# Kernel optimization log

Hardware: AMD Instinct MI355X
Metric: run time of the kernel (lower is better)

## Reference

```python
import jax, jax.numpy as jnp
import numpy as np

TOP_K = 4

def setup_inputs() -> dict:
    key = jax.random.key(0)
    ks = jax.random.split(key, 10)
    s = 0.02
    return {
        "x": jax.random.normal(ks[0], (4, 1024, 2048), jnp.float32),
        "expert_bias": jnp.zeros((64,), jnp.float32),
        "router_w": jax.random.normal(ks[1], (64, 2048), jnp.float32) * s,
        "gate_w": jax.random.normal(ks[2], (8192, 2048), jnp.float32) * s,
        "up_w": jax.random.normal(ks[3], (8192, 2048), jnp.float32) * s,
        "down_w": jax.random.normal(ks[4], (2048, 8192), jnp.float32) * s,
        "w_down": jax.random.normal(ks[5], (512, 2048), jnp.float32) * s,
        "w_up": jax.random.normal(ks[6], (2048, 512), jnp.float32) * s,
        "experts_w12": jax.random.normal(ks[7], (64, 512, 2048), jnp.float32) * s,
        "experts_w3": jax.random.normal(ks[8], (64, 1024, 512), jnp.float32) * s,
    }


def reference(x, expert_bias, router_w, gate_w, up_w, down_w, w_down, w_up, experts_w12, experts_w3):
    B, S, D = x.shape
    E = router_w.shape[0]
    K = TOP_K
    h = x.reshape(-1, D)            # [N, D]
    N = h.shape[0]
    NK = N * K

    # --- router (fp32) ---
    logits = h @ router_w.T          # [N, E]
    scores = jax.nn.sigmoid(logits)
    z_loss = jnp.mean(logits * logits) * 1e-4
    sel = scores + expert_bias
    _, topk_idx = jax.lax.top_k(sel, K)                      # [N, K]
    topk_logits = jnp.take_along_axis(logits, topk_idx, axis=1)
    gating = jax.nn.softmax(topk_logits, axis=-1)            # [N, K]

    # --- shared SwiGLU expert ---
    shared = (jax.nn.silu(h @ gate_w.T) * (h @ up_w.T)) @ down_w.T   # [N, D]

    # --- bottleneck down projection ---
    hd = h @ w_down.T                # [N, bottle]
    Bn = hd.shape[1]

    # --- dispatch: sort tokens by expert, capacity max_load per expert ---
    flat = topk_idx.reshape(-1)                      # [NK]
    perm = jnp.argsort(flat)                         # stable sort
    sorted_e = flat[perm]
    counts = jnp.bincount(flat, length=E)
    ptr = jnp.cumsum(counts) - counts                # start offset per expert
    local = jnp.arange(NK) - ptr[sorted_e]           # rank within expert
    max_load = (NK // E // 8 + 6) * 8                # static python int
    num_slots = E * max_load
    mask = local < max_load
    slots = sorted_e * max_load + local
    tok = jnp.repeat(jnp.arange(N), K)               # token id per routed slot

    # reverse_map[slot] = token index (N = dummy)
    rm = jnp.full((num_slots + 1,), N, dtype=jnp.int32)
    rm = rm.at[jnp.where(mask, slots, num_slots)].set(tok[perm].astype(jnp.int32))
    reverse_map = rm[:num_slots]

    hwd = jnp.concatenate([hd, jnp.zeros((1, Bn), hd.dtype)], axis=0)
    padding = hwd[reverse_map].reshape(E, max_load, Bn)

    # --- grouped expert GEMMs ---
    h12 = jnp.einsum('emb,ebf->emf', padding, experts_w12)   # [E, L, 2*F]
    h1, h2 = jnp.split(h12, 2, axis=-1)
    pout = jnp.einsum('emf,efb->emb', jax.nn.silu(h1) * h2, experts_w3)
    pout = pout.reshape(-1, Bn)                              # [num_slots, bottle]

    # --- combine: gather back per (token, k) slot and mix with gating ---
    powd = jnp.concatenate([pout, jnp.zeros((1, Bn), pout.dtype)], axis=0)
    gm = jnp.full((NK + 1,), num_slots, dtype=jnp.int32)
    gm = gm.at[jnp.where(mask, perm, NK)].set(jnp.where(mask, slots, num_slots).astype(jnp.int32))
    gather_map = gm[:NK]
    gathered = powd[gather_map].reshape(N, K, Bn)
    routed_b = jnp.einsum('nk,nkb->nb', gating, gathered)
    routed = routed_b @ w_up.T                               # [N, D]

    # eval mode: route_scale = 1.0, moe_scale = 0.5 (one shared expert), aux_loss = 0
    out = (shared + routed) * 0.5
    return out.reshape(B, S, D), z_loss
```

## Files before the change

kernel.cpp:

```cpp
#include <hip/hip_runtime.h>
#include <math.h>

#define NTOK 4096
#define DMODEL 2048
#define ENUM 64
#define HSH 8192
#define BND 512
#define FEXP 1024
#define MAXL 304
#define EPAD 384
#define ECH 16

typedef float f32x4 __attribute__((ext_vector_type(4)));
using bf16x8 = __attribute__((ext_vector_type(8))) __bf16;

typedef const __attribute__((address_space(1))) unsigned int cgu32;
typedef __attribute__((address_space(3))) unsigned int lu32;
#define GLOAD16(g, l) __builtin_amdgcn_global_load_lds((cgu32*)(g), (lu32*)(l), 16, 0, 0)

__device__ __forceinline__ unsigned short f2bf(float f) {
    union { float f; unsigned int u; } v; v.f = f;
    unsigned int u = v.u;
    return (unsigned short)((u + 0x7FFFu + ((u >> 16) & 1u)) >> 16);
}
__device__ __forceinline__ float bf2f(unsigned short s) {
    union { unsigned int u; float f; } v; v.u = ((unsigned int)s) << 16;
    return v.f;
}

__global__ __launch_bounds__(256) void init_kernel(float* zacc, int* slot2tok, unsigned short* hdz) {
    int i = blockIdx.x * 256 + threadIdx.x;
    if (i == 0) *zacc = 0.f;
    if (i < ENUM * MAXL) slot2tok[i] = NTOK;
    if (i < BND) hdz[i] = 0;
}

__global__ __launch_bounds__(256) void convert_kernel(
    const float* __restrict__ in, unsigned short* __restrict__ out, long long n)
{
    long long stride = (long long)gridDim.x * 256 * 8;
    for (long long i = ((long long)blockIdx.x * 256 + threadIdx.x) * 8; i < n; i += stride) {
        float4 a = *(const float4*)(in + i);
        float4 b = *(const float4*)(in + i + 4);
        union { unsigned short s[8]; uint4 v; } o;
        o.s[0] = f2bf(a.x); o.s[1] = f2bf(a.y); o.s[2] = f2bf(a.z); o.s[3] = f2bf(a.w);
        o.s[4] = f2bf(b.x); o.s[5] = f2bf(b.y); o.s[6] = f2bf(b.z); o.s[7] = f2bf(b.w);
        *(uint4*)(out + i) = o.v;
    }
}

__global__ __launch_bounds__(256) void convert_x_kernel(
    const float* __restrict__ in, unsigned short* __restrict__ hi,
    unsigned short* __restrict__ lo, long long n)
{
    long long stride = (long long)gridDim.x * 256 * 8;
    for (long long i = ((long long)blockIdx.x * 256 + threadIdx.x) * 8; i < n; i += stride) {
        float4 a = *(const float4*)(in + i);
        float4 b = *(const float4*)(in + i + 4);
        union { unsigned short s[8]; uint4 v; } oh, ol;
        float f[8] = {a.x, a.y, a.z, a.w, b.x, b.y, b.z, b.w};
#pragma unroll
        for (int j = 0; j < 8; j++) {
            unsigned short h = f2bf(f[j]);
            oh.s[j] = h;
            ol.s[j] = f2bf(f[j] - bf2f(h));
        }
        *(uint4*)(hi + i) = oh.v;
        *(uint4*)(lo + i) = ol.v;
    }
}

__global__ __launch_bounds__(256) void convert_rw_kernel(
    const float* __restrict__ rw, unsigned short* __restrict__ whi,
    unsigned short* __restrict__ wlo)
{
    int i = (blockIdx.x * 256 + threadIdx.x) * 4;
    if (i >= 128 * 2048) return;
    ushort4 oh = {0, 0, 0, 0}, ol = {0, 0, 0, 0};
    if (i < 64 * 2048) {
        float4 f = *(const float4*)(rw + i);
        float v[4] = {f.x, f.y, f.z, f.w};
        unsigned short h;
        h = f2bf(v[0]); oh.x = h; ol.x = f2bf(v[0] - bf2f(h));
        h = f2bf(v[1]); oh.y = h; ol.y = f2bf(v[1] - bf2f(h));
        h = f2bf(v[2]); oh.z = h; ol.z = f2bf(v[2] - bf2f(h));
        h = f2bf(v[3]); oh.w = h; ol.w = f2bf(v[3] - bf2f(h));
    }
    *(ushort4*)(whi + i) = oh;
    *(ushort4*)(wlo + i) = ol;
}

__global__ __launch_bounds__(256) void tconv_kernel(
    const float* __restrict__ in, unsigned short* __restrict__ out, int Kd, int Nd)
{
    __shared__ float t[32][33];
    size_t zoff = (size_t)blockIdx.z * Kd * Nd;
    in += zoff; out += zoff;
    int n0 = blockIdx.x * 32, k0 = blockIdx.y * 32;
    int r = threadIdx.x >> 3, c = (threadIdx.x & 7) * 4;
    float4 v = *(const float4*)(in + (size_t)(k0 + r) * Nd + n0 + c);
    t[r][c] = v.x; t[r][c + 1] = v.y; t[r][c + 2] = v.z; t[r][c + 3] = v.w;
    __syncthreads();
    ushort4 o;
    o.x = f2bf(t[c + 0][r]); o.y = f2bf(t[c + 1][r]);
    o.z = f2bf(t[c + 2][r]); o.w = f2bf(t[c + 3][r]);
    *(ushort4*)(out + (size_t)(n0 + r) * Kd + k0 + c) = o;
}

__global__ __launch_bounds__(256) void rgemm_kernel(
    const unsigned short* __restrict__ xb, const unsigned short* __restrict__ xlo,
    const unsigned short* __restrict__ whi, const unsigned short* __restrict__ wlo,
    float* __restrict__ logits)
{
    __shared__ unsigned short As[2][128 * 64];
    __shared__ unsigned short Bs[2][128 * 64];
    const int z = blockIdx.z;
    const int m0 = blockIdx.y * 128;
    const int tid = threadIdx.x;
    const int lane = tid & 63;
    const int w = tid >> 6;
    const int wm = (w >> 1) * 64;
    const int wn = (w & 1) * 64;

    const unsigned short* Ab = (z == 2) ? xlo : xb;
    const unsigned short* Bb = (z == 1) ? wlo : whi;
    float* Cb = logits + (size_t)z * NTOK * 128;

    size_t asrc[4], bsrc[4];
    int ldso[4];
#pragma unroll
    for (int i = 0; i < 4; i++) {
        int u = i * 256 + tid;
        int r = u >> 3;
        int ce = ((u & 7) ^ (r & 7)) * 8;
        ldso[i] = u * 8;
        asrc[i] = (size_t)(m0 + r) * DMODEL + ce;
        bsrc[i] = (size_t)r * DMODEL + ce;
    }

    const int lrow = lane & 15;
    const int kg = lane >> 4;
    const int mk = (lrow & 7) << 4;
    int arx[4], brx[4];
#pragma unroll
    for (int t = 0; t < 4; t++) {
        arx[t] = (wm + t * 16 + lrow) * 128;
        brx[t] = (wn + t * 16 + lrow) * 128;
    }

    f32x4 acc[4][4];
#pragma unroll
    for (int a = 0; a < 4; a++)
#pragma unroll
        for (int b = 0; b < 4; b++) acc[a][b] = (f32x4)0.f;

#pragma unroll
    for (int i = 0; i < 4; i++) GLOAD16(Ab + asrc[i], &As[0][ldso[i]]);
#pragma unroll
    for (int i = 0; i < 4; i++) GLOAD16(Bb + bsrc[i], &Bs[0][ldso[i]]);
#pragma unroll
    for (int i = 0; i < 4; i++) GLOAD16(Ab + asrc[i] + 64, &As[1][ldso[i]]);
#pragma unroll
    for (int i = 0; i < 4; i++) GLOAD16(Bb + bsrc[i] + 64, &Bs[1][ldso[i]]);

    const int nt = DMODEL >> 6;
    int cur = 0;
    for (int t = 0; t < nt; ++t) {
        if (t + 1 < nt) asm volatile("s_waitcnt vmcnt(8)" ::: "memory");
        else            asm volatile("s_waitcnt vmcnt(0)" ::: "memory");
        __builtin_amdgcn_s_barrier();
        __builtin_amdgcn_sched_barrier(0);
        const char* Abase = (const char*)&As[cur][0];
        const char* Bbase = (const char*)&Bs[cur][0];
#pragma unroll
        for (int ks = 0; ks < 2; ks++) {
            const int cb = (ks * 64 + kg * 16) ^ mk;
            bf16x8 a[4], b[4];
#pragma unroll
            for (int t2 = 0; t2 < 4; t2++) {
                a[t2] = *(const bf16x8*)(Abase + arx[t2] + cb);
                b[t2] = *(const bf16x8*)(Bbase + brx[t2] + cb);
            }
#pragma unroll
            for (int ni = 0; ni < 4; ni++)
#pragma unroll
                for (int mi = 0; mi < 4; mi++)
                    acc[mi][ni] = __builtin_amdgcn_mfma_f32_16x16x32_bf16(a[mi], b[ni], acc[mi][ni], 0, 0, 0);
        }
        __builtin_amdgcn_sched_barrier(0);
        asm volatile("s_waitcnt lgkmcnt(0)" ::: "memory");
        __builtin_amdgcn_s_barrier();
        __builtin_amdgcn_sched_barrier(0);
        const int kn = (t + 2) * 64;
        if (kn < DMODEL) {
#pragma unroll
            for (int i = 0; i < 4; i++) GLOAD16(Ab + asrc[i] + kn, &As[cur][ldso[i]]);
#pragma unroll
            for (int i = 0; i < 4; i++) GLOAD16(Bb + bsrc[i] + kn, &Bs[cur][ldso[i]]);
        }
        cur ^= 1;
    }

    const int rb0 = m0 + wm + (kg << 2);
#pragma unroll
    for (int mi = 0; mi < 4; mi++)
#pragma unroll
        for (int ni = 0; ni < 4; ni++) {
            int col = wn + ni * 16 + lrow;
#pragma unroll
            for (int r = 0; r < 4; r++)
                Cb[(size_t)(rb0 + mi * 16 + r) * 128 + col] = acc[mi][ni][r];
        }
}

__global__ __launch_bounds__(256) void topk_kernel(
    const float* __restrict__ logits, const float* __restrict__ bias,
    int* __restrict__ topk_idx, float* __restrict__ gating, float* __restrict__ zacc)
{
    __shared__ float zpart[4];
    const size_t Z = (size_t)NTOK * 128;
    int wv = threadIdx.x >> 6, lane = threadIdx.x & 63;
    int n = blockIdx.x * 4 + wv;
    const float* lp = logits + (size_t)n * 128 + lane;
    float logit = lp[0] + lp[Z] + lp[2 * Z];
    float sel = 1.f / (1.f + expf(-logit)) + bias[lane];
    float zsq = logit * logit;
    for (int off = 32; off; off >>= 1) zsq += __shfl_down(zsq, off);
    if (lane == 0) zpart[wv] = zsq;
    __syncthreads();
    if (threadIdx.x == 0) atomicAdd(zacc, zpart[0] + zpart[1] + zpart[2] + zpart[3]);
    float cur = sel;
    float ch_logit[4]; int ch_idx[4];
    for (int kk = 0; kk < 4; kk++) {
        float v = cur; int idx = lane;
        for (int off = 1; off < 64; off <<= 1) {
            float v2 = __shfl_xor(v, off);
            int i2 = __shfl_xor(idx, off);
            if (v2 > v || (v2 == v && i2 < idx)) { v = v2; idx = i2; }
        }
        ch_idx[kk] = idx;
        ch_logit[kk] = __shfl(logit, idx);
        if (lane == idx) cur = -1e30f;
    }
    if (lane == 0) {
        float mx = ch_logit[0];
        for (int kk = 1; kk < 4; kk++) mx = fmaxf(mx, ch_logit[kk]);
        float se = 0.f, ex[4];
        for (int kk = 0; kk < 4; kk++) { ex[kk] = expf(ch_logit[kk] - mx); se += ex[kk]; }
        for (int kk = 0; kk < 4; kk++) {
            topk_idx[n * 4 + kk] = ch_idx[kk];
            gating[n * 4 + kk] = ex[kk] / se;
        }
    }
}

__global__ __launch_bounds__(256) void rank_kernel(
    const int* __restrict__ topk_idx, int* __restrict__ slot2tok, int* __restrict__ gmap)
{
    int e = blockIdx.x;
    __shared__ int wsum[4];
    int tid = threadIdx.x;
    int lane = tid & 63, w = tid >> 6;
    int running = 0;
    for (int c = 0; c < NTOK * 4; c += 256) {
        int i = c + tid;
        int fl = topk_idx[i];
        bool m = (fl == e);
        unsigned long long bal = __ballot(m);
        int prefix = __popcll(bal & ((1ULL << lane) - 1ULL));
        if (lane == 0) wsum[w] = __popcll(bal);
        __syncthreads();
        int wbase = 0;
        for (int j = 0; j < w; j++) wbase += wsum[j];
        int total = wsum[0] + wsum[1] + wsum[2] + wsum[3];
        if (m) {
            int rank = running + wbase + prefix;
            int tok = i >> 2;
            if (rank < MAXL) {
                slot2tok[e * MAXL + rank] = tok;
                gmap[i] = e * MAXL + rank;
            } else gmap[i] = -1;
        }
        running += total;
        __syncthreads();
    }
}

template<int GATHER, int EPI>
__global__ __launch_bounds__(256) void gemm2(
    const unsigned short* __restrict__ A, long long aZ, int lda,
    const int* __restrict__ gtab,
    const unsigned short* __restrict__ Bm, long long bZ, int ldb,
    void* __restrict__ Cb, long long cZ, int ldc,
    int M, int K)
{
    __shared__ unsigned short As[2][128 * 64];
    __shared__ unsigned short Bs[2][128 * 64];
    const int z = blockIdx.z;
    const int m0 = blockIdx.y * 128;
    const int n0 = blockIdx.x * 128;
    const int tid = threadIdx.x;
    const int lane = tid & 63;
    const int w = tid >> 6;
    const int wm = (w >> 1) * 64;
    const int wn = (w & 1) * 64;

    const unsigned short* Ab = A + (GATHER ? (size_t)0 : (size_t)z * aZ);
    const unsigned short* Bb = Bm + (size_t)z * bZ;

    size_t asrc[4], bsrc[4];
    int ldso[4];
#pragma unroll
    for (int i = 0; i < 4; i++) {
        int u = i * 256 + tid;
        int r = u >> 3;
        int ce = ((u & 7) ^ (r & 7)) * 8;
        ldso[i] = u * 8;
        if constexpr (GATHER) {
            int mr = m0 + r;
            int tok = (mr < M) ? gtab[(size_t)z * MAXL + mr] : NTOK;
            asrc[i] = (size_t)tok * lda + ce;
        } else {
            asrc[i] = (size_t)(m0 + r) * lda + ce;
        }
        bsrc[i] = (size_t)(n0 + r) * ldb + ce;
    }

    const int lrow = lane & 15;
    const int kg = lane >> 4;
    const int mk = (lrow & 7) << 4;
    int arx[4], brx[4];
#pragma unroll
    for (int t = 0; t < 4; t++) {
        arx[t] = (wm + t * 16 + lrow) * 128;
        brx[t] = (wn + t * 16 + lrow) * 128;
    }

    f32x4 acc[4][4];
#pragma unroll
    for (int a = 0; a < 4; a++)
#pragma unroll
        for (int b = 0; b < 4; b++) acc[a][b] = (f32x4)0.f;

#pragma unroll
    for (int i = 0; i < 4; i++) GLOAD16(Ab + asrc[i], &As[0][ldso[i]]);
#pragma unroll
    for (int i = 0; i < 4; i++) GLOAD16(Bb + bsrc[i], &Bs[0][ldso[i]]);
    if (64 < K) {
#pragma unroll
        for (int i = 0; i < 4; i++) GLOAD16(Ab + asrc[i] + 64, &As[1][ldso[i]]);
#pragma unroll
        for (int i = 0; i < 4; i++) GLOAD16(Bb + bsrc[i] + 64, &Bs[1][ldso[i]]);
    }

    const int nt = K >> 6;
    int cur = 0;
    for (int t = 0; t < nt; ++t) {
        if (t + 1 < nt) asm volatile("s_waitcnt vmcnt(8)" ::: "memory");
        else            asm volatile("s_waitcnt vmcnt(0)" ::: "memory");
        __builtin_amdgcn_s_barrier();
        __builtin_amdgcn_sched_barrier(0);
        const char* Abase = (const char*)&As[cur][0];
        const char* Bbase = (const char*)&Bs[cur][0];
#pragma unroll
        for (int ks = 0; ks < 2; ks++) {
            const int cb = (ks * 64 + kg * 16) ^ mk;
            bf16x8 a[4], b[4];
#pragma unroll
            for (int t2 = 0; t2 < 4; t2++) {
                a[t2] = *(const bf16x8*)(Abase + arx[t2] + cb);
                b[t2] = *(const bf16x8*)(Bbase + brx[t2] + cb);
            }
#pragma unroll
            for (int ni = 0; ni < 4; ni++)
#pragma unroll
                for (int mi = 0; mi < 4; mi++)
                    acc[mi][ni] = __builtin_amdgcn_mfma_f32_16x16x32_bf16(a[mi], b[ni], acc[mi][ni], 0, 0, 0);
        }
        __builtin_amdgcn_sched_barrier(0);
        asm volatile("s_waitcnt lgkmcnt(0)" ::: "memory");
        __builtin_amdgcn_s_barrier();
        __builtin_amdgcn_sched_barrier(0);
        const int kn = (t + 2) * 64;
        if (kn < K) {
#pragma unroll
            for (int i = 0; i < 4; i++) GLOAD16(Ab + asrc[i] + kn, &As[cur][ldso[i]]);
#pragma unroll
            for (int i = 0; i < 4; i++) GLOAD16(Bb + bsrc[i] + kn, &Bs[cur][ldso[i]]);
        }
        cur ^= 1;
    }

    const int rb0 = m0 + wm + (kg << 2);
#pragma unroll
    for (int mi = 0; mi < 4; mi++)
#pragma unroll
        for (int ni = 0; ni < 4; ni++) {
            int col = n0 + wn + ni * 16 + lrow;
#pragma unroll
            for (int r = 0; r < 4; r++) {
                int row = rb0 + mi * 16 + r;
                if (row < M) {
                    size_t ci = (size_t)z * cZ + (size_t)row * ldc + col;
                    float v = acc[mi][ni][r];
                    if constexpr (EPI == 0) {
                        ((unsigned short*)Cb)[ci] = f2bf(v);
                    } else if constexpr (EPI == 1) {
                        unsigned short* cp = (unsigned short*)Cb + ci;
                        float g = bf2f(*cp);
                        *cp = f2bf(g / (1.f + expf(-g)) * v);
                    } else if constexpr (EPI == 2) {
                        ((float*)Cb)[ci] = v;
                    } else {
                        float* cp = (float*)Cb + ci;
                        *cp = (*cp + v) * 0.5f;
                    }
                }
            }
        }
}

__global__ __launch_bounds__(256) void siluact_kernel(
    const unsigned short* __restrict__ h12, unsigned short* __restrict__ act)
{
    int e = blockIdx.y, m = blockIdx.x;
    const unsigned short* hr = h12 + ((size_t)e * EPAD + m) * 2048;
    unsigned short* ar = act + ((size_t)e * EPAD + m) * 1024;
    int j = threadIdx.x * 4;
    ushort4 h1 = *(const ushort4*)(hr + j);
    ushort4 h2 = *(const ushort4*)(hr + 1024 + j);
    ushort4 o;
    float v;
    v = bf2f(h1.x); o.x = f2bf(v / (1.f + expf(-v)) * bf2f(h2.x));
    v = bf2f(h1.y); o.y = f2bf(v / (1.f + expf(-v)) * bf2f(h2.y));
    v = bf2f(h1.z); o.z = f2bf(v / (1.f + expf(-v)) * bf2f(h2.z));
    v = bf2f(h1.w); o.w = f2bf(v / (1.f + expf(-v)) * bf2f(h2.w));
    *(ushort4*)(ar + j) = o;
}

__global__ __launch_bounds__(256) void gather_kernel(
    const unsigned short* __restrict__ pout, const int* __restrict__ gmap,
    const float* __restrict__ gating, unsigned short* __restrict__ routed_b)
{
    int n = blockIdx.x;
    int j = threadIdx.x * 2;
    float a0 = 0.f, a1 = 0.f;
#pragma unroll
    for (int kk = 0; kk < 4; kk++) {
        int slot = gmap[n * 4 + kk];
        float g = gating[n * 4 + kk];
        if (slot >= 0) {
            const unsigned short* pr = pout + (size_t)slot * BND + j;
            a0 += g * bf2f(pr[0]);
            a1 += g * bf2f(pr[1]);
        }
    }
    routed_b[(size_t)n * BND + j] = f2bf(a0);
    routed_b[(size_t)n * BND + j + 1] = f2bf(a1);
}

__global__ void zloss_kernel(const float* zacc, float* out) {
    out[0] = zacc[0] * (1.0e-4f / (float)(NTOK * ENUM));
}

extern "C" void kernel_launch(void* const* d_in, const int* in_sizes, int n_in,
                              void* d_out, int out_size, void* d_ws, size_t ws_size,
                              hipStream_t stream)
{
    const float* x      = (const float*)d_in[0];
    const float* ebias  = (const float*)d_in[1];
    const float* rw     = (const float*)d_in[2];
    const float* gate_w = (const float*)d_in[3];
    const float* up_w   = (const float*)d_in[4];
    const float* down_w = (const float*)d_in[5];
    const float* w_down = (const float*)d_in[6];
    const float* w_up   = (const float*)d_in[7];
    const float* w12    = (const float*)d_in[8];
    const float* w3     = (const float*)d_in[9];
    float* out = (float*)d_out;

    char* ws = (char*)d_ws;
    size_t off = 0;
    auto alloc = [&](size_t b) { size_t o = off; off += (b + 255) & ~(size_t)255; return o; };
    float* zacc     = (float*)(ws + alloc(4));
    int*   topk     = (int*)(ws + alloc((size_t)NTOK * 4 * 4));
    float* gating   = (float*)(ws + alloc((size_t)NTOK * 4 * 4));
    int*   gmap     = (int*)(ws + alloc((size_t)NTOK * 4 * 4));
    int*   slot2tok = (int*)(ws + alloc((size_t)ENUM * MAXL * 4));
    unsigned short* xb     = (unsigned short*)(ws + alloc((size_t)NTOK * DMODEL * 2));
    unsigned short* hd     = (unsigned short*)(ws + alloc((size_t)(NTOK + 1) * BND * 2));
    unsigned short* rb     = (unsigned short*)(ws + alloc((size_t)NTOK * BND * 2));
    unsigned short* wdownb = (unsigned short*)(ws + alloc((size_t)BND * DMODEL * 2));
    unsigned short* wupb   = (unsigned short*)(ws + alloc((size_t)DMODEL * BND * 2));
    unsigned short* wbuf   = (unsigned short*)(ws + alloc((size_t)HSH * DMODEL * 2));
    unsigned short* H1     = (unsigned short*)(ws + alloc((size_t)NTOK * HSH * 2));
    unsigned short* h12  = H1;
    unsigned short* act  = H1 + (size_t)ECH * EPAD * 2048;
    unsigned short* pout = H1 + (size_t)ECH * EPAD * 2048 + (size_t)ECH * EPAD * 1024;
    unsigned short* xlo    = H1;
    float*          logits = (float*)((char*)H1 + (size_t)NTOK * DMODEL * 2);
    unsigned short* whi    = (unsigned short*)((char*)logits + (size_t)3 * NTOK * 128 * 4);
    unsigned short* wlo    = whi + (size_t)128 * DMODEL;

    init_kernel<<<(ENUM * MAXL + 255) / 256, 256, 0, stream>>>(zacc, slot2tok, hd + (size_t)NTOK * BND);

    convert_x_kernel<<<1024, 256, 0, stream>>>(x, xb, xlo, (long long)NTOK * DMODEL);
    convert_rw_kernel<<<(128 * 2048 / 4 + 255) / 256, 256, 0, stream>>>(rw, whi, wlo);
    rgemm_kernel<<<dim3(1, NTOK / 128, 3), 256, 0, stream>>>(xb, xlo, whi, wlo, logits);
    topk_kernel<<<NTOK / 4, 256, 0, stream>>>(logits, ebias, topk, gating, zacc);
    rank_kernel<<<ENUM, 256, 0, stream>>>(topk, slot2tok, gmap);

    convert_kernel<<<256, 256, 0, stream>>>(w_down, wdownb, (long long)BND * DMODEL);
    convert_kernel<<<256, 256, 0, stream>>>(w_up, wupb, (long long)DMODEL * BND);

    gemm2<0, 0><<<dim3(BND / 128, NTOK / 128, 1), 256, 0, stream>>>(
        xb, 0, DMODEL, nullptr, wdownb, 0, DMODEL, hd, 0, BND, NTOK, DMODEL);

    convert_kernel<<<1024, 256, 0, stream>>>(gate_w, wbuf, (long long)HSH * DMODEL);
    gemm2<0, 0><<<dim3(HSH / 128, NTOK / 128, 1), 256, 0, stream>>>(
        xb, 0, DMODEL, nullptr, wbuf, 0, DMODEL, H1, 0, HSH, NTOK, DMODEL);
    convert_kernel<<<1024, 256, 0, stream>>>(up_w, wbuf, (long long)HSH * DMODEL);
    gemm2<0, 1><<<dim3(HSH / 128, NTOK / 128, 1), 256, 0, stream>>>(
        xb, 0, DMODEL, nullptr, wbuf, 0, DMODEL, H1, 0, HSH, NTOK, DMODEL);
    convert_kernel<<<1024, 256, 0, stream>>>(down_w, wbuf, (long long)DMODEL * HSH);
    gemm2<0, 2><<<dim3(DMODEL / 128, NTOK / 128, 1), 256, 0, stream>>>(
        H1, 0, HSH, nullptr, wbuf, 0, HSH, out, 0, DMODEL, NTOK, HSH);

    for (int c = 0; c < ENUM / ECH; c++) {
        tconv_kernel<<<dim3(2048 / 32, 512 / 32, ECH), 256, 0, stream>>>(
            w12 + (size_t)c * ECH * 512 * 2048, wbuf, 512, 2048);
        gemm2<1, 0><<<dim3(2048 / 128, 3, ECH), 256, 0, stream>>>(
            hd, 0, BND, slot2tok + (size_t)c * ECH * MAXL,
            wbuf, (long long)2048 * 512, 512,
            h12, (long long)EPAD * 2048, 2048, MAXL, BND);
        tconv_kernel<<<dim3(512 / 32, 1024 / 32, ECH), 256, 0, stream>>>(
            w3 + (size_t)c * ECH * 1024 * 512, wbuf, 1024, 512);
        siluact_kernel<<<dim3(EPAD, ECH), 256, 0, stream>>>(h12, act);
        gemm2<0, 0><<<dim3(BND / 128, 3, ECH), 256, 0, stream>>>(
            act, (long long)EPAD * FEXP, FEXP, nullptr,
            wbuf, (long long)BND * FEXP, FEXP,
            pout + (size_t)c * ECH * MAXL * BND, (long long)MAXL * BND, BND, MAXL, FEXP);
    }

    gather_kernel<<<NTOK, 256, 0, stream>>>(pout, gmap, gating, rb);

    gemm2<0, 3><<<dim3(DMODEL / 128, NTOK / 128, 1), 256, 0, stream>>>(
        rb, 0, BND, nullptr, wupb, 0, BND, out, 0, DMODEL, NTOK, BND);

    zloss_kernel<<<1, 1, 0, stream>>>(zacc, out + (size_t)NTOK * DMODEL);
}
```

Baseline: 1.097 ms.

## Fuse shared-expert gate and up GEMMs into one dual-accumulator kernel

Replaces the separate gate GEMM (bf16 store) and up GEMM (read-back plus SiLU epilogue) with a single kernel. It loads one A tile and both gate and up B tiles, keeps two accumulator sets, and writes silu(g)*u directly. This reads the activation tiles once and avoids writing and re-reading the intermediate H1 gate result. Weights are converted in two halves so they fit the existing buffer. The cost is much higher register use (32 f32x4 accumulators) and 48KB of LDS per block, which may lower occupancy.

```diff
diff --git a/kernel.cpp b/kernel.cpp
--- a/kernel.cpp
+++ b/kernel.cpp
@@ -420,6 +420,95 @@
         }
 }
 
+__global__ __launch_bounds__(256) void gemmgu(
+    const unsigned short* __restrict__ A, int lda,
+    const unsigned short* __restrict__ Bg, const unsigned short* __restrict__ Bu,
+    int ldb, unsigned short* __restrict__ H, int ldh, int ncol0, int K)
+{
+    __shared__ unsigned short As[128 * 64];
+    __shared__ unsigned short Bgs[128 * 64];
+    __shared__ unsigned short Bus[128 * 64];
+    const int m0 = blockIdx.y * 128;
+    const int n0 = blockIdx.x * 128;
+    const int tid = threadIdx.x;
+    const int lane = tid & 63;
+    const int w = tid >> 6;
+    const int wm = (w >> 1) * 64;
+    const int wn = (w & 1) * 64;
+
+    size_t asrc[4], bsrc[4];
+    int ldso[4];
+#pragma unroll
+    for (int i = 0; i < 4; i++) {
+        int u = i * 256 + tid;
+        int r = u >> 3;
+        int ce = ((u & 7) ^ (r & 7)) * 8;
+        ldso[i] = u * 8;
+        asrc[i] = (size_t)(m0 + r) * lda + ce;
+        bsrc[i] = (size_t)(n0 + r) * ldb + ce;
+    }
+
+    const int lrow = lane & 15;
+    const int kg = lane >> 4;
+    const int mk = (lrow & 7) << 4;
+    int arx[4], brx[4];
+#pragma unroll
+    for (int t = 0; t < 4; t++) {
+        arx[t] = (wm + t * 16 + lrow) * 128;
+        brx[t] = (wn + t * 16 + lrow) * 128;
+    }
+
+    f32x4 accg[4][4], accu[4][4];
+#pragma unroll
+    for (int a = 0; a < 4; a++)
+#pragma unroll
+        for (int b = 0; b < 4; b++) { accg[a][b] = (f32x4)0.f; accu[a][b] = (f32x4)0.f; }
+
+    for (int k0 = 0; k0 < K; k0 += 64) {
+#pragma unroll
+        for (int i = 0; i < 4; i++) GLOAD16(A + asrc[i] + k0, &As[ldso[i]]);
+#pragma unroll
+        for (int i = 0; i < 4; i++) GLOAD16(Bg + bsrc[i] + k0, &Bgs[ldso[i]]);
+#pragma unroll
+        for (int i = 0; i < 4; i++) GLOAD16(Bu + bsrc[i] + k0, &Bus[ldso[i]]);
+        __syncthreads();
+#pragma unroll
+        for (int ks = 0; ks < 2; ks++) {
+            const int cb = (ks * 64 + kg * 16) ^ mk;
+            bf16x8 a[4], bg[4], bu[4];
+#pragma unroll
+            for (int t2 = 0; t2 < 4; t2++) {
+                a[t2]  = *(const bf16x8*)((const char*)As  + arx[t2] + cb);
+                bg[t2] = *(const bf16x8*)((const char*)Bgs + brx[t2] + cb);
+                bu[t2] = *(const bf16x8*)((const char*)Bus + brx[t2] + cb);
+            }
+#pragma unroll
+            for (int ni = 0; ni < 4; ni++)
+#pragma unroll
+                for (int mi = 0; mi < 4; mi++) {
+                    accg[mi][ni] = __builtin_amdgcn_mfma_f32_16x16x32_bf16(a[mi], bg[ni], accg[mi][ni], 0, 0, 0);
+                    accu[mi][ni] = __builtin_amdgcn_mfma_f32_16x16x32_bf16(a[mi], bu[ni], accu[mi][ni], 0, 0, 0);
+                }
+        }
+        __syncthreads();
+    }
+
+    const int rb0 = m0 + wm + (kg << 2);
+#pragma unroll
+    for (int mi = 0; mi < 4; mi++)
+#pragma unroll
+        for (int ni = 0; ni < 4; ni++) {
+            int col = ncol0 + n0 + wn + ni * 16 + lrow;
+#pragma unroll
+            for (int r = 0; r < 4; r++) {
+                int row = rb0 + mi * 16 + r;
+                float g = accg[mi][ni][r];
+                float u = accu[mi][ni][r];
+                H[(size_t)row * ldh + col] = f2bf(g / (1.f + expf(-g)) * u);
+            }
+        }
+}
+
 __global__ __launch_bounds__(256) void siluact_kernel(
     const unsigned short* __restrict__ h12, unsigned short* __restrict__ act)
 {
@@ -516,12 +605,16 @@
     gemm2<0, 0><<<dim3(BND / 128, NTOK / 128, 1), 256, 0, stream>>>(
         xb, 0, DMODEL, nullptr, wdownb, 0, DMODEL, hd, 0, BND, NTOK, DMODEL);
 
-    convert_kernel<<<1024, 256, 0, stream>>>(gate_w, wbuf, (long long)HSH * DMODEL);
-    gemm2<0, 0><<<dim3(HSH / 128, NTOK / 128, 1), 256, 0, stream>>>(
-        xb, 0, DMODEL, nullptr, wbuf, 0, DMODEL, H1, 0, HSH, NTOK, DMODEL);
-    convert_kernel<<<1024, 256, 0, stream>>>(up_w, wbuf, (long long)HSH * DMODEL);
-    gemm2<0, 1><<<dim3(HSH / 128, NTOK / 128, 1), 256, 0, stream>>>(
-        xb, 0, DMODEL, nullptr, wbuf, 0, DMODEL, H1, 0, HSH, NTOK, DMODEL);
+    for (int half = 0; half < 2; half++) {
+        convert_kernel<<<512, 256, 0, stream>>>(
+            gate_w + (size_t)half * (HSH / 2) * DMODEL, wbuf, (long long)(HSH / 2) * DMODEL);
+        convert_kernel<<<512, 256, 0, stream>>>(
+            up_w + (size_t)half * (HSH / 2) * DMODEL, wbuf + (size_t)(HSH / 2) * DMODEL,
+            (long long)(HSH / 2) * DMODEL);
+        gemmgu<<<dim3((HSH / 2) / 128, NTOK / 128, 1), 256, 0, stream>>>(
+            xb, DMODEL, wbuf, wbuf + (size_t)(HSH / 2) * DMODEL, DMODEL,
+            H1, HSH, half * (HSH / 2), DMODEL);
+    }
     convert_kernel<<<1024, 256, 0, stream>>>(down_w, wbuf, (long long)DMODEL * HSH);
     gemm2<0, 2><<<dim3(DMODEL / 128, NTOK / 128, 1), 256, 0, stream>>>(
         H1, 0, HSH, nullptr, wbuf, 0, HSH, out, 0, DMODEL, NTOK, HSH);
```

Measured after the change: 1.184 ms. +7.9%, slower.

## Add 256x256-tile triple-buffered bf16 GEMM for shared expert gate/up projections

Applied to the files above, without the earlier changes.

Introduces a new GEMM kernel with 256x256 output tiles, 512 threads (8 waves, each 128x64), a three-stage LDS ring filled by direct global-to-LDS loads, and XOR-swizzled LDS layout. It replaces the 128x128 gemm2 for the two large shared-expert gate and up projections (4096x8192x2048). The goal is higher arithmetic intensity per LDS byte and better latency hiding on the dominant GEMMs. The cost is higher register and LDS use (about 96KB LDS, 128 accumulator floats per thread), which lowers occupancy, plus fewer blocks (512) across the CUs.

```diff
diff --git a/kernel.cpp b/kernel.cpp
--- a/kernel.cpp
+++ b/kernel.cpp
@@ -420,6 +420,116 @@
         }
 }
 
+template<int EPI>
+__global__ __launch_bounds__(512) void gemm3(
+    const unsigned short* __restrict__ A, int lda,
+    const unsigned short* __restrict__ Bm, int ldb,
+    unsigned short* __restrict__ C, int ldc, int K)
+{
+    __shared__ unsigned short As[3][256 * 32];
+    __shared__ unsigned short Bs[3][256 * 32];
+    const int m0 = blockIdx.y * 256;
+    const int n0 = blockIdx.x * 256;
+    const int tid = threadIdx.x;
+    const int lane = tid & 63;
+    const int w = tid >> 6;
+    const int wm = (w >> 2) * 128;
+    const int wn = (w & 3) * 64;
+
+    size_t asrc[2], bsrc[2];
+    int ldso[2];
+#pragma unroll
+    for (int i = 0; i < 2; i++) {
+        int u = i * 512 + tid;
+        int r = u >> 2;
+        int ce = ((u & 3) ^ ((r >> 1) & 3)) * 8;
+        ldso[i] = u * 8;
+        asrc[i] = (size_t)(m0 + r) * lda + ce;
+        bsrc[i] = (size_t)(n0 + r) * ldb + ce;
+    }
+
+    const int lrow = lane & 15;
+    const int kg = lane >> 4;
+    const int un = (kg ^ ((lrow >> 1) & 3)) << 4;
+    int arx[8], brx[4];
+#pragma unroll
+    for (int mi = 0; mi < 8; mi++) arx[mi] = (wm + mi * 16 + lrow) * 64 + un;
+#pragma unroll
+    for (int ni = 0; ni < 4; ni++) brx[ni] = (wn + ni * 16 + lrow) * 64 + un;
+
+    f32x4 acc[8][4];
+#pragma unroll
+    for (int a = 0; a < 8; a++)
+#pragma unroll
+        for (int b = 0; b < 4; b++) acc[a][b] = (f32x4)0.f;
+
+#pragma unroll
+    for (int i = 0; i < 2; i++) GLOAD16(A + asrc[i], &As[0][ldso[i]]);
+#pragma unroll
+    for (int i = 0; i < 2; i++) GLOAD16(Bm + bsrc[i], &Bs[0][ldso[i]]);
+#pragma unroll
+    for (int i = 0; i < 2; i++) GLOAD16(A + asrc[i] + 32, &As[1][ldso[i]]);
+#pragma unroll
+    for (int i = 0; i < 2; i++) GLOAD16(Bm + bsrc[i] + 32, &Bs[1][ldso[i]]);
+
+    const int nt = K >> 5;
+    int cur = 0;
+    for (int t = 0; t < nt; ++t) {
+        if (t + 1 < nt) asm volatile("s_waitcnt vmcnt(4)" ::: "memory");
+        else            asm volatile("s_waitcnt vmcnt(0)" ::: "memory");
+        __builtin_amdgcn_s_barrier();
+        __builtin_amdgcn_sched_barrier(0);
+        if (t + 2 < nt) {
+            int nb = cur + 2; if (nb >= 3) nb -= 3;
+            const int kn = (t + 2) * 32;
+#pragma unroll
+            for (int i = 0; i < 2; i++) GLOAD16(A + asrc[i] + kn, &As[nb][ldso[i]]);
+#pragma unroll
+            for (int i = 0; i < 2; i++) GLOAD16(Bm + bsrc[i] + kn, &Bs[nb][ldso[i]]);
+        }
+        const char* Abase = (const char*)&As[cur][0];
+        const char* Bbase = (const char*)&Bs[cur][0];
+        bf16x8 a[8], b[4];
+#pragma unroll
+        for (int mi = 0; mi < 8; mi++) a[mi] = *(const bf16x8*)(Abase + arx[mi]);
+#pragma unroll
+        for (int ni = 0; ni < 4; ni++) b[ni] = *(const bf16x8*)(Bbase + brx[ni]);
+        __builtin_amdgcn_s_setprio(1);
+#pragma unroll
+        for (int ni = 0; ni < 4; ni++)
+#pragma unroll
+            for (int mi = 0; mi < 8; mi++)
+                acc[mi][ni] = __builtin_amdgcn_mfma_f32_16x16x32_bf16(a[mi], b[ni], acc[mi][ni], 0, 0, 0);
+        __builtin_amdgcn_s_setprio(0);
+        __builtin_amdgcn_sched_barrier(0);
+        asm volatile("s_waitcnt lgkmcnt(0)" ::: "memory");
+        __builtin_amdgcn_s_barrier();
+        __builtin_amdgcn_sched_barrier(0);
+        cur += 1; if (cur >= 3) cur -= 3;
+    }
+
+    const int rb0 = m0 + wm + (kg << 2);
+#pragma unroll
+    for (int mi = 0; mi < 8; mi++)
+#pragma unroll
+        for (int ni = 0; ni < 4; ni++) {
+            int col = n0 + wn + ni * 16 + lrow;
+#pragma unroll
+            for (int r = 0; r < 4; r++) {
+                int row = rb0 + mi * 16 + r;
+                size_t ci = (size_t)row * ldc + col;
+                float v = acc[mi][ni][r];
+                if constexpr (EPI == 0) {
+                    C[ci] = f2bf(v);
+                } else {
+                    unsigned short* cp = C + ci;
+                    float g = bf2f(*cp);
+                    *cp = f2bf(g / (1.f + expf(-g)) * v);
+                }
+            }
+        }
+}
+
 __global__ __launch_bounds__(256) void siluact_kernel(
     const unsigned short* __restrict__ h12, unsigned short* __restrict__ act)
 {
@@ -517,11 +627,11 @@
         xb, 0, DMODEL, nullptr, wdownb, 0, DMODEL, hd, 0, BND, NTOK, DMODEL);
 
     convert_kernel<<<1024, 256, 0, stream>>>(gate_w, wbuf, (long long)HSH * DMODEL);
-    gemm2<0, 0><<<dim3(HSH / 128, NTOK / 128, 1), 256, 0, stream>>>(
-        xb, 0, DMODEL, nullptr, wbuf, 0, DMODEL, H1, 0, HSH, NTOK, DMODEL);
+    gemm3<0><<<dim3(HSH / 256, NTOK / 256), 512, 0, stream>>>(
+        xb, DMODEL, wbuf, DMODEL, H1, HSH, DMODEL);
     convert_kernel<<<1024, 256, 0, stream>>>(up_w, wbuf, (long long)HSH * DMODEL);
-    gemm2<0, 1><<<dim3(HSH / 128, NTOK / 128, 1), 256, 0, stream>>>(
-        xb, 0, DMODEL, nullptr, wbuf, 0, DMODEL, H1, 0, HSH, NTOK, DMODEL);
+    gemm3<1><<<dim3(HSH / 256, NTOK / 256), 512, 0, stream>>>(
+        xb, DMODEL, wbuf, DMODEL, H1, HSH, DMODEL);
     convert_kernel<<<1024, 256, 0, stream>>>(down_w, wbuf, (long long)DMODEL * HSH);
     gemm2<0, 2><<<dim3(DMODEL / 128, NTOK / 128, 1), 256, 0, stream>>>(
         H1, 0, HSH, nullptr, wbuf, 0, HSH, out, 0, DMODEL, NTOK, HSH);
```

After: 1.124 ms. +2.5%, slower.
